# Optimization experiments

Measured on AMD Instinct MI355X. Metric: run time of the kernel, lower is better.

The kernel has to match this reference:

```python
import jax, jax.numpy as jnp
import numpy as np

EPS = 1e-5
N_HEADS = 16

def _bn(x, g, b, m, v):
    # x: (N,C,L); inference-mode batchnorm with running stats
    scale = g * jax.lax.rsqrt(v + EPS)
    return (x - m[None, :, None]) * scale[None, :, None] + b[None, :, None]

def _conv1d(x, w, b, pad):
    # x: (N,C,L), w: (O,I,K) torch layout
    y = jax.lax.conv_general_dilated(x, w, window_strides=(1,), padding=[(pad, pad)],
                                     dimension_numbers=('NCH', 'OIH', 'NCH'))
    return y + b[None, :, None]

def _instance_norm(x):
    m = x.mean(-1, keepdims=True)
    v = x.var(-1, keepdims=True)
    return (x - m) * jax.lax.rsqrt(v + EPS)

def setup_inputs() -> dict:
    key = jax.random.key(0)
    ks = jax.random.split(key, 12)
    C, MID, N, L = 1024, 1024, 4, 1024
    s = 0.02
    d = {
        'x': jax.random.normal(ks[0], (N, C, L), jnp.float32),
        'norm_g': jnp.ones((C,), jnp.float32) + 0.1 * jax.random.normal(ks[1], (C,)),
        'norm_b': 0.1 * jax.random.normal(ks[2], (C,)),
        'norm_m': 0.05 * jax.random.normal(ks[3], (C,)),
        'norm_v': jnp.ones((C,), jnp.float32),
        'wq': s * jax.random.normal(ks[4], (C, C)),
        'wk': s * jax.random.normal(ks[5], (C, C)),
        'wv': s * jax.random.normal(ks[6], (C, C)),
        'wo': s * jax.random.normal(ks[7], (C, C)),
        'cw1': s * jax.random.normal(ks[8], (MID, C, 1)),
        'cb1': jnp.zeros((MID,), jnp.float32),
        'cw2': s * jax.random.normal(ks[9], (MID, MID, 3)),
        'cb2': jnp.zeros((MID,), jnp.float32),
        'cw3': s * jax.random.normal(ks[10], (C, MID, 1)),
        'cb3': jnp.zeros((C,), jnp.float32),
    }
    for i, cdim in [(1, MID), (2, MID), (3, C)]:
        kk = jax.random.split(ks[11], 8)
        d[f'bn{i}_g'] = jnp.ones((cdim,), jnp.float32) + 0.1 * jax.random.normal(kk[2 * i - 2], (cdim,))
        d[f'bn{i}_b'] = 0.1 * jax.random.normal(kk[2 * i - 1], (cdim,))
        d[f'bn{i}_m'] = 0.05 * jax.random.normal(jax.random.fold_in(key, 100 + i), (cdim,))
        d[f'bn{i}_v'] = jnp.ones((cdim,), jnp.float32)
    return d

def _attention(h, wq, wk, wv, wo):
    # h: (N,L,C) ; torch Linear: y = x @ W.T
    N, L, C = h.shape
    dh = C // N_HEADS
    q = (h @ wq.T).reshape(N, L, N_HEADS, dh)
    k = (h @ wk.T).reshape(N, L, N_HEADS, dh)
    v = (h @ wv.T).reshape(N, L, N_HEADS, dh)
    att = jnp.einsum('nqhd,nkhd->nhqk', q, k) / jnp.sqrt(jnp.float32(C))  # note: /sqrt(d_model) as in source
    att = jax.nn.softmax(att, axis=-1)
    o = jnp.einsum('nhqk,nkhd->nqhd', att, v).reshape(N, L, C)
    return o @ wo.T

def _forward(x, norm_g, norm_b, norm_m, norm_v, wq, wk, wv, wo,
             cw1, cb1, bn1_g, bn1_b, bn1_m, bn1_v,
             cw2, cb2, bn2_g, bn2_b, bn2_m, bn2_v,
             cw3, cb3, bn3_g, bn3_b, bn3_m, bn3_v):
    # self-attention branch (dropout is identity in eval)
    h = _bn(x, norm_g, norm_b, norm_m, norm_v).transpose(0, 2, 1)  # (N,L,C)
    h = h + _attention(h, wq, wk, wv, wo)
    h = h.transpose(0, 2, 1)  # (N,C,L)
    # IbnNet (bottleneck conv block + residual + optional InstanceNorm)
    y = jax.nn.relu(_bn(_conv1d(h, cw1, cb1, 0), bn1_g, bn1_b, bn1_m, bn1_v))
    y = jax.nn.relu(_bn(_conv1d(y, cw2, cb2, 1), bn2_g, bn2_b, bn2_m, bn2_v))
    y = _bn(_conv1d(y, cw3, cb3, 0), bn3_g, bn3_b, bn3_m, bn3_v)
    y = jax.nn.relu(_instance_norm(y + h))
    # max_pool1d(kernel=2, stride=2)
    N, C, L = y.shape
    return y.reshape(N, C, L // 2, 2).max(axis=-1)

def reference(x, norm_g, norm_b, norm_m, norm_v, wq, wk, wv, wo,
              cw1, cb1, bn1_g, bn1_b, bn1_m, bn1_v,
              cw2, cb2, bn2_g, bn2_b, bn2_m, bn2_v,
              cw3, cb3, bn3_g, bn3_b, bn3_m, bn3_v):
    return _forward(x, norm_g, norm_b, norm_m, norm_v, wq, wk, wv, wo,
                    cw1, cb1, bn1_g, bn1_b, bn1_m, bn1_v,
                    cw2, cb2, bn2_g, bn2_b, bn2_m, bn2_v,
                    cw3, cb3, bn3_g, bn3_b, bn3_m, bn3_v)
```

## Files before the change

kernel.cpp:

```cpp
#include <hip/hip_runtime.h>
#include <cstdint>
#include <cstddef>


typedef __bf16 bf16_t;
typedef __attribute__((ext_vector_type(8))) __bf16 bf16x8;
typedef __attribute__((ext_vector_type(4))) __bf16 bf16x4;
typedef __attribute__((ext_vector_type(4))) float f32x4;
typedef __attribute__((ext_vector_type(8))) unsigned short u16x8;
typedef __attribute__((address_space(1))) unsigned int gu32;
typedef __attribute__((address_space(3))) unsigned int lu32;

#define EPSF 1e-5f

__device__ __forceinline__ void glds16(const void* g, void* l) {
  __builtin_amdgcn_global_load_lds((gu32*)g, (lu32*)l, 16, 0, 0);
}

__device__ __forceinline__ f32x4 mfma16(bf16x8 a, bf16x8 b, f32x4 c) {
  return __builtin_amdgcn_mfma_f32_16x16x32_bf16(a, b, c, 0, 0, 0);
}

struct BnAll {
  const float *g0, *b0, *m0, *v0;
  const float *g1, *b1, *m1, *v1, *cb1;
  const float *g2, *b2, *m2, *v2, *cb2;
  const float *g3, *b3, *m3, *v3, *cb3;
};
__global__ void bn_consts4_k(BnAll a, float* __restrict__ base) {
  const int sec = blockIdx.x >> 2;
  const int i = (blockIdx.x & 3) * 256 + threadIdx.x;
  const float *g, *b, *m, *v, *cb;
  switch (sec) {
    case 0: g = a.g0; b = a.b0; m = a.m0; v = a.v0; cb = nullptr; break;
    case 1: g = a.g1; b = a.b1; m = a.m1; v = a.v1; cb = a.cb1; break;
    case 2: g = a.g2; b = a.b2; m = a.m2; v = a.v2; cb = a.cb2; break;
    default: g = a.g3; b = a.b3; m = a.m3; v = a.v3; cb = a.cb3; break;
  }
  float s = g[i] * rsqrtf(v[i] + EPSF);
  base[sec * 2048 + i] = s;
  base[sec * 2048 + 1024 + i] = b[i] + ((cb ? cb[i] : 0.f) - m[i]) * s;
}

__global__ __launch_bounds__(256)
void bn_transpose_k(const float* __restrict__ x, const float* __restrict__ sc,
                    const float* __restrict__ sh, bf16_t* __restrict__ H0b) {
  __shared__ float T[32][33];
  const int n = blockIdx.x, c0 = blockIdx.y * 32, l0 = blockIdx.z * 32;
  const int tx = threadIdx.x & 31, ty = threadIdx.x >> 5;
#pragma unroll
  for (int cc = 0; cc < 4; ++cc) {
    int c = c0 + ty + cc * 8;
    float v = x[((size_t)(n * 1024 + c) << 10) + l0 + tx];
    T[ty + cc * 8][tx] = v * sc[c] + sh[c];
  }
  __syncthreads();
#pragma unroll
  for (int cc = 0; cc < 4; ++cc) {
    int l = l0 + ty + cc * 8;
    float v = T[tx][ty + cc * 8];
    H0b[((size_t)(n * 1024 + l) << 10) + c0 + tx] = (bf16_t)v;
  }
}

__global__ void prep_w_k(const float* __restrict__ s0, const float* __restrict__ s1,
                         const float* __restrict__ s2, const float* __restrict__ s3,
                         const float* __restrict__ s4, const float* __restrict__ s5,
                         const float* __restrict__ w2s,
                         bf16_t* __restrict__ d0, bf16_t* __restrict__ d1,
                         bf16_t* __restrict__ d2, bf16_t* __restrict__ d3,
                         bf16_t* __restrict__ d4, bf16_t* __restrict__ d5,
                         bf16_t* __restrict__ w2d) {
  const int b = blockIdx.x;
  if (b < 6144) {
    const int which = b >> 10;
    const int i = (b & 1023) * 256 + threadIdx.x;
    const float* s; bf16_t* d;
    switch (which) {
      case 0: s = s0; d = d0; break;
      case 1: s = s1; d = d1; break;
      case 2: s = s2; d = d2; break;
      case 3: s = s3; d = d3; break;
      case 4: s = s4; d = d4; break;
      default: s = s5; d = d5; break;
    }
    f32x4 v = *(const f32x4*)(s + (size_t)i * 4);
    bf16x4 o;
    o[0] = (bf16_t)v[0]; o[1] = (bf16_t)v[1]; o[2] = (bf16_t)v[2]; o[3] = (bf16_t)v[3];
    *(bf16x4*)(d + (size_t)i * 4) = o;
  } else {
    const int j0 = ((b - 6144) * 256 + (int)threadIdx.x) * 4;
    const int o = j0 / 3072;
    const int r = j0 - o * 3072;
    const int t = r >> 10;
    const int c0 = r & 1023;
    const float* src = w2s + (size_t)o * 3072 + t;
    bf16x4 ov;
#pragma unroll
    for (int e = 0; e < 4; ++e) ov[e] = (bf16_t)src[(c0 + e) * 3];
    *(bf16x4*)(w2d + (size_t)j0) = ov;
  }
}

__global__ void zero_y1p_pads_k(bf16_t* __restrict__ Y1p) {
  int i = blockIdx.x * 256 + threadIdx.x;
  int n = i >> 11, r = (i >> 10) & 1, c = i & 1023;
  Y1p[(size_t)(n * 1026 + (r ? 1025 : 0)) * 1024 + c] = (bf16_t)0.f;
}

__global__ __launch_bounds__(256)
void gemm_nt(const bf16_t* __restrict__ A, const bf16_t* __restrict__ B, int K,
             int lda, int ldb, int aPad, int outPad, int nNT, int qkv,
             const float* __restrict__ bnScale, const float* __restrict__ bnShift,
             int doRelu, const bf16_t* __restrict__ residB,
             bf16_t* __restrict__ outB, float* __restrict__ statS,
             float* __restrict__ statQ) {
  __shared__ __align__(16) bf16_t As[2][128 * 64];
  __shared__ __align__(16) bf16_t Bs[2][64 * 64];
  __shared__ float SrS[2][2][16], SrQ[2][2][16];

  const int bid = blockIdx.x;
  const int wg = (bid & 7) * (gridDim.x >> 3) + (bid >> 3);
  const int mt = wg / nNT, nt = wg - mt * nNT;
  const int tileM = mt * 128, tileN = nt * 64;

  const int tid = threadIdx.x;
  const int lane = tid & 63;
  const int w = tid >> 6, wr = w >> 1, wc = w & 1;
  const int l16 = lane & 15, g = lane >> 4;

  const bf16_t* aSrc[4];
  const bf16_t* bSrc[2];
#pragma unroll
  for (int it = 0; it < 4; ++it) {
    int q = it * 256 + tid, r = q >> 3, s = q & 7;
    int ar = tileM + r;
    if (aPad) ar = (ar >> 10) * 1026 + (ar & 1023);
    aSrc[it] = A + (size_t)ar * lda + ((s ^ (r & 7)) * 8);
  }
#pragma unroll
  for (int it = 0; it < 2; ++it) {
    int q = it * 256 + tid, r = q >> 3, s = q & 7;
    bSrc[it] = B + (size_t)(tileN + r) * ldb + ((s ^ (r & 7)) * 8);
  }

  f32x4 acc[4][2];
#pragma unroll
  for (int m = 0; m < 4; ++m)
#pragma unroll
    for (int n = 0; n < 2; ++n) acc[m][n] = {0.f, 0.f, 0.f, 0.f};

#pragma unroll
  for (int it = 0; it < 4; ++it) glds16(aSrc[it], &As[0][(it * 256 + tid) * 8]);
#pragma unroll
  for (int it = 0; it < 2; ++it) glds16(bSrc[it], &Bs[0][(it * 256 + tid) * 8]);
  __syncthreads();

  int buf = 0;
  for (int k0 = 0; k0 < K; k0 += 64) {
    if (k0 + 64 < K) {
#pragma unroll
      for (int it = 0; it < 4; ++it)
        glds16(aSrc[it] + k0 + 64, &As[buf ^ 1][(it * 256 + tid) * 8]);
#pragma unroll
      for (int it = 0; it < 2; ++it)
        glds16(bSrc[it] + k0 + 64, &Bs[buf ^ 1][(it * 256 + tid) * 8]);
    }
#pragma unroll
    for (int kk = 0; kk < 2; ++kk) {
      bf16x8 af[4], bfr[2];
#pragma unroll
      for (int m = 0; m < 4; ++m) {
        int r = wr * 64 + m * 16 + l16;
        af[m] = *(const bf16x8*)(&As[buf][r * 64 + (((kk * 4 + g) ^ (r & 7)) * 8)]);
      }
#pragma unroll
      for (int n = 0; n < 2; ++n) {
        int r = wc * 32 + n * 16 + l16;
        bfr[n] = *(const bf16x8*)(&Bs[buf][r * 64 + (((kk * 4 + g) ^ (r & 7)) * 8)]);
      }
#pragma unroll
      for (int m = 0; m < 4; ++m)
#pragma unroll
        for (int n = 0; n < 2; ++n) acc[m][n] = mfma16(af[m], bfr[n], acc[m][n]);
    }
    __syncthreads();
    buf ^= 1;
  }

  float sA[2] = {0.f, 0.f}, qA[2] = {0.f, 0.f};
#pragma unroll
  for (int m = 0; m < 4; ++m) {
#pragma unroll
    for (int n = 0; n < 2; ++n) {
#pragma unroll
      for (int j = 0; j < 4; ++j) {
        const int gr = tileM + wr * 64 + m * 16 + g * 4 + j;
        const int gc = tileN + wc * 32 + n * 16 + l16;
        if (qkv) {
          const int which = gc >> 10, c = gc & 1023;
          float v = acc[m][n][j] * (which == 0 ? 0.03125f : 1.f);
          if (which == 2)
            outB[8388608 + ((size_t)(gr >> 10) << 20) + ((size_t)c << 10) + (gr & 1023)] =
                (bf16_t)v;
          else
            outB[(size_t)which * 4194304 + ((size_t)gr << 10) + c] = (bf16_t)v;
        } else {
          float v = acc[m][n][j];
          if (bnScale) v = v * bnScale[gc] + bnShift[gc];
          if (residB) v += (float)residB[((size_t)gr << 10) + gc];
          if (doRelu) v = fmaxf(v, 0.f);
          size_t orow = gr;
          if (outPad) orow = (size_t)((gr >> 10) * 1026 + (gr & 1023) + 1);
          outB[orow * 1024 + gc] = (bf16_t)v;
          if (statS) { sA[n] += v; qA[n] += v * v; }
        }
      }
    }
  }

  if (statS) {
#pragma unroll
    for (int n = 0; n < 2; ++n) {
      sA[n] += __shfl_xor(sA[n], 16); sA[n] += __shfl_xor(sA[n], 32);
      qA[n] += __shfl_xor(qA[n], 16); qA[n] += __shfl_xor(qA[n], 32);
    }
    if (wr == 1 && lane < 16) {
      SrS[wc][0][lane] = sA[0]; SrS[wc][1][lane] = sA[1];
      SrQ[wc][0][lane] = qA[0]; SrQ[wc][1][lane] = qA[1];
    }
    __syncthreads();
    if (wr == 0 && lane < 16) {
      const int z = mt & 7, nb = mt >> 3;
#pragma unroll
      for (int n = 0; n < 2; ++n) {
        const int gc = tileN + wc * 32 + n * 16 + lane;
        statS[z * 4096 + nb * 1024 + gc] = sA[n] + SrS[wc][n][lane];
        statQ[z * 4096 + nb * 1024 + gc] = qA[n] + SrQ[wc][n][lane];
      }
    }
  }
}

__global__ __launch_bounds__(256)
void attn_fwd(const bf16_t* __restrict__ Qb, const bf16_t* __restrict__ Kb,
              const bf16_t* __restrict__ Vt, bf16_t* __restrict__ AO) {
  __shared__ __align__(16) bf16_t Ks[2][64][64];
  __shared__ __align__(16) bf16_t Vs[2][64][64];
  __shared__ __align__(16) bf16_t Ps[4][2][16][64];

  const int bid = blockIdx.x;
  const int xcd = bid & 7, idx = bid >> 3;
  const int head = xcd * 8 + (idx >> 3);
  const int qblk = idx & 7;
  const int n = head >> 4, h = head & 15;

  const int tid = threadIdx.x, lane = tid & 63, w = tid >> 6;
  const int l16 = lane & 15, g = lane >> 4;
  const int qbase = qblk * 128 + w * 32;

  bf16x8 aq[2][2];
#pragma unroll
  for (int s = 0; s < 2; ++s) {
    const size_t qoff = ((size_t)(n * 1024 + qbase + s * 16 + l16) << 10) + h * 64;
    aq[s][0] = *(const bf16x8*)(Qb + qoff + g * 8);
    aq[s][1] = *(const bf16x8*)(Qb + qoff + 32 + g * 8);
  }

  const bf16_t* Khead = Kb + ((size_t)(n * 1024) << 10) + h * 64;
  const bf16_t* Vhead = Vt + ((size_t)n << 20) + ((size_t)(h * 64) << 10);

  f32x4 oa[2][4];
  float psum[2][4];
#pragma unroll
  for (int s = 0; s < 2; ++s)
#pragma unroll
    for (int i = 0; i < 4; ++i) {
      oa[s][i] = {0.f, 0.f, 0.f, 0.f};
      psum[s][i] = 0.f;
    }

#pragma unroll
  for (int it = 0; it < 2; ++it) {
    int q = it * 256 + tid, r = q >> 3, c = q & 7;
    glds16(Khead + ((size_t)r << 10) + ((c ^ (r & 7)) * 8), &Ks[0][r][c * 8]);
    glds16(Vhead + ((size_t)r << 10) + ((c ^ (r & 7)) * 8), &Vs[0][r][c * 8]);
  }
  asm volatile("s_waitcnt vmcnt(0)" ::: "memory");
  __syncthreads();

  int buf = 0;
  for (int t = 0; t < 16; ++t) {
    if (t < 15) {
      const int kv0 = (t + 1) * 64;
#pragma unroll
      for (int it = 0; it < 2; ++it) {
        int q = it * 256 + tid, r = q >> 3, c = q & 7;
        glds16(Khead + ((size_t)(kv0 + r) << 10) + ((c ^ (r & 7)) * 8),
               &Ks[buf ^ 1][r][c * 8]);
        glds16(Vhead + ((size_t)r << 10) + kv0 + ((c ^ (r & 7)) * 8),
               &Vs[buf ^ 1][r][c * 8]);
      }
    }
    bf16x8 kf[8];
#pragma unroll
    for (int nf = 0; nf < 4; ++nf) {
      const int r = nf * 16 + l16;
      kf[2 * nf]     = *(const bf16x8*)(&Ks[buf][r][((g)     ^ (r & 7)) * 8]);
      kf[2 * nf + 1] = *(const bf16x8*)(&Ks[buf][r][((4 + g) ^ (r & 7)) * 8]);
    }
#pragma unroll
    for (int s = 0; s < 2; ++s) {
      f32x4 sc[4];
#pragma unroll
      for (int nf = 0; nf < 4; ++nf) sc[nf] = {0.f, 0.f, 0.f, 0.f};
#pragma unroll
      for (int nf = 0; nf < 4; ++nf) {
        sc[nf] = mfma16(aq[s][0], kf[2 * nf], sc[nf]);
        sc[nf] = mfma16(aq[s][1], kf[2 * nf + 1], sc[nf]);
      }
#pragma unroll
      for (int nf = 0; nf < 4; ++nf)
#pragma unroll
        for (int j = 0; j < 4; ++j) {
          float p = __expf(sc[nf][j]);
          psum[s][j] += p;
          const int row = g * 4 + j;
          const int ch = (nf * 2 + (l16 >> 3)) ^ (row & 7);
          Ps[w][s][row][ch * 8 + (l16 & 7)] = (bf16_t)p;
        }
    }
    bf16x8 vf[8];
#pragma unroll
    for (int nf = 0; nf < 4; ++nf) {
      const int r = nf * 16 + l16;
      vf[2 * nf]     = *(const bf16x8*)(&Vs[buf][r][((g)     ^ (r & 7)) * 8]);
      vf[2 * nf + 1] = *(const bf16x8*)(&Vs[buf][r][((4 + g) ^ (r & 7)) * 8]);
    }
#pragma unroll
    for (int s = 0; s < 2; ++s)
#pragma unroll
      for (int kk = 0; kk < 2; ++kk) {
        const int ch = (kk * 4 + g) ^ (l16 & 7);
        bf16x8 pa = *(const bf16x8*)(&Ps[w][s][l16][ch * 8]);
#pragma unroll
        for (int nf = 0; nf < 4; ++nf)
          oa[s][nf] = mfma16(pa, vf[2 * nf + kk], oa[s][nf]);
      }
    asm volatile("s_waitcnt vmcnt(0)" ::: "memory");
    __syncthreads();
    buf ^= 1;
  }

#pragma unroll
  for (int s = 0; s < 2; ++s)
#pragma unroll
    for (int j = 0; j < 4; ++j) {
      float sv = psum[s][j];
#pragma unroll
      for (int o = 1; o < 16; o <<= 1) sv += __shfl_xor(sv, o);
      psum[s][j] = sv;
    }
#pragma unroll
  for (int s = 0; s < 2; ++s)
#pragma unroll
    for (int nf = 0; nf < 4; ++nf)
#pragma unroll
      for (int j = 0; j < 4; ++j) {
        const int q = qbase + s * 16 + g * 4 + j;
        AO[((size_t)(n * 1024 + q) << 10) + h * 64 + nf * 16 + l16] =
            (bf16_t)(oa[s][nf][j] / psum[s][j]);
      }
}

__global__ __launch_bounds__(256)
void finalize_k(const bf16_t* __restrict__ Z, const float* __restrict__ ps,
                const float* __restrict__ pq, float* __restrict__ out) {
  __shared__ float T[32][33];
  const int n = blockIdx.x, c0 = blockIdx.y * 32, j0 = blockIdx.z * 32;
  const int tx = threadIdx.x & 31, ty = threadIdx.x >> 5;
  const int c = c0 + tx;
  float s = 0.f, q = 0.f;
#pragma unroll
  for (int z = 0; z < 8; ++z) {
    s += ps[z * 4096 + n * 1024 + c];
    q += pq[z * 4096 + n * 1024 + c];
  }
  const float mean = s * (1.f / 1024.f);
  const float var = q * (1.f / 1024.f) - mean * mean;
  const float rstd = rsqrtf(var + EPSF);
#pragma unroll
  for (int jj = 0; jj < 4; ++jj) {
    const int j = j0 + ty + jj * 8;
    float a = (float)Z[((size_t)(n * 1024 + 2 * j) << 10) + c];
    float b = (float)Z[((size_t)(n * 1024 + 2 * j + 1) << 10) + c];
    float v = (fmaxf(a, b) - mean) * rstd;
    T[ty + jj * 8][tx] = fmaxf(v, 0.f);
  }
  __syncthreads();
#pragma unroll
  for (int jj = 0; jj < 4; ++jj)
    out[((size_t)(n * 1024 + c0 + ty + jj * 8) << 9) + j0 + tx] = T[tx][ty + jj * 8];
}

extern "C" void kernel_launch(void* const* d_in, const int* in_sizes, int n_in,
                              void* d_out, int out_size, void* d_ws, size_t ws_size,
                              hipStream_t stream) {
  const float* x      = (const float*)d_in[0];
  const float* norm_g = (const float*)d_in[1];
  const float* norm_b = (const float*)d_in[2];
  const float* norm_m = (const float*)d_in[3];
  const float* norm_v = (const float*)d_in[4];
  const float* wq     = (const float*)d_in[5];
  const float* wk     = (const float*)d_in[6];
  const float* wv     = (const float*)d_in[7];
  const float* wo     = (const float*)d_in[8];
  const float* cw1    = (const float*)d_in[9];
  const float* cb1    = (const float*)d_in[10];
  const float* cw2    = (const float*)d_in[11];
  const float* cb2    = (const float*)d_in[12];
  const float* cw3    = (const float*)d_in[13];
  const float* cb3    = (const float*)d_in[14];
  const float* bn1_g  = (const float*)d_in[15];
  const float* bn1_b  = (const float*)d_in[16];
  const float* bn1_m  = (const float*)d_in[17];
  const float* bn1_v  = (const float*)d_in[18];
  const float* bn2_g  = (const float*)d_in[19];
  const float* bn2_b  = (const float*)d_in[20];
  const float* bn2_m  = (const float*)d_in[21];
  const float* bn2_v  = (const float*)d_in[22];
  const float* bn3_g  = (const float*)d_in[23];
  const float* bn3_b  = (const float*)d_in[24];
  const float* bn3_m  = (const float*)d_in[25];
  const float* bn3_v  = (const float*)d_in[26];

  char* ws = (char*)d_ws;
  const size_t MB = 1024 * 1024;
  bf16_t* Zb  = (bf16_t*)(ws);
  bf16_t* H0b = (bf16_t*)(ws + 32 * MB);
  bf16_t* Y2  = H0b;
  bf16_t* Qb  = (bf16_t*)(ws + 40 * MB);
  bf16_t* Kb  = (bf16_t*)(ws + 48 * MB);
  bf16_t* Vt  = (bf16_t*)(ws + 56 * MB);
  bf16_t* Y1p = Qb;
  bf16_t* AOb = (bf16_t*)(ws + 64 * MB);
  bf16_t* H2b = (bf16_t*)(ws + 72 * MB);
  bf16_t* wqb = (bf16_t*)(ws + 80 * MB);
  bf16_t* wkb = (bf16_t*)(ws + 82 * MB);
  bf16_t* wvb = (bf16_t*)(ws + 84 * MB);
  bf16_t* wob = (bf16_t*)(ws + 86 * MB);
  bf16_t* w1b = (bf16_t*)(ws + 88 * MB);
  bf16_t* w3b = (bf16_t*)(ws + 90 * MB);
  bf16_t* w2b = (bf16_t*)(ws + 92 * MB);
  float* cb   = (float*)(ws + 98 * MB);
  float* sc0 = cb,        * sh0 = cb + 1024;
  float* sc1 = cb + 2048, * sh1 = cb + 3072;
  float* sc2 = cb + 4096, * sh2 = cb + 5120;
  float* sc3 = cb + 6144, * sh3 = cb + 7168;
  float* ps  = cb + 8192;
  float* pq  = ps + 32768;

  BnAll ba = {norm_g, norm_b, norm_m, norm_v,
              bn1_g, bn1_b, bn1_m, bn1_v, cb1,
              bn2_g, bn2_b, bn2_m, bn2_v, cb2,
              bn3_g, bn3_b, bn3_m, bn3_v, cb3};
  bn_consts4_k<<<16, 256, 0, stream>>>(ba, cb);

  bn_transpose_k<<<dim3(4, 32, 32), 256, 0, stream>>>(x, sc0, sh0, H0b);

  prep_w_k<<<9216, 256, 0, stream>>>(wq, wk, wv, wo, cw1, cw3, cw2,
                                     wqb, wkb, wvb, wob, w1b, w3b, w2b);

  gemm_nt<<<1536, 256, 0, stream>>>(H0b, wqb, 1024, 1024, 1024, 0, 0, 48, 1,
                                    nullptr, nullptr, 0, nullptr, Qb,
                                    nullptr, nullptr);

  attn_fwd<<<512, 256, 0, stream>>>(Qb, Kb, Vt, AOb);

  zero_y1p_pads_k<<<32, 256, 0, stream>>>(Y1p);

  gemm_nt<<<512, 256, 0, stream>>>(AOb, wob, 1024, 1024, 1024, 0, 0, 16, 0,
                                   nullptr, nullptr, 0, H0b, H2b,
                                   nullptr, nullptr);
  gemm_nt<<<512, 256, 0, stream>>>(H2b, w1b, 1024, 1024, 1024, 0, 1, 16, 0,
                                   sc1, sh1, 1, nullptr, Y1p,
                                   nullptr, nullptr);
  gemm_nt<<<512, 256, 0, stream>>>(Y1p, w2b, 3072, 1024, 3072, 1, 0, 16, 0,
                                   sc2, sh2, 1, nullptr, Y2,
                                   nullptr, nullptr);
  gemm_nt<<<512, 256, 0, stream>>>(Y2, w3b, 1024, 1024, 1024, 0, 0, 16, 0,
                                   sc3, sh3, 0, H2b, Zb, ps, pq);

  finalize_k<<<dim3(4, 32, 16), 256, 0, stream>>>(Zb, ps, pq, (float*)d_out);
}
```

Baseline: 246.8 us.

## Add dedicated 256x256-tile pipelined QKV GEMM kernel with 8 waves

```diff
diff --git a/kernel.cpp b/kernel.cpp
--- a/kernel.cpp
+++ b/kernel.cpp
@@ -108,9 +108,135 @@
   Y1p[(size_t)(n * 1026 + (r ? 1025 : 0)) * 1024 + c] = (bf16_t)0.f;
 }
 
+__global__ __launch_bounds__(512, 2)
+void gemm_qkv8(const bf16_t* __restrict__ A, const bf16_t* __restrict__ B,
+               bf16_t* __restrict__ out) {
+  __shared__ __align__(16) bf16_t As[2][2][8192];
+  __shared__ __align__(16) bf16_t Bs[2][2][8192];
+
+  const int bid = blockIdx.x;
+  const int wg = (bid & 7) * 24 + (bid >> 3);
+  const int mt = wg / 12, nt = wg - mt * 12;
+  const int tileM = mt * 256, tileN = nt * 256;
+
+  const int tid = threadIdx.x;
+  const int lane = tid & 63;
+  const int w = tid >> 6;
+  const int wm = w >> 2, wn = w & 3;
+  const int l16 = lane & 15, gg = lane >> 4;
+  const int bhalf = wn >> 1, bbase = (wn & 1) * 64;
+
+  const bf16_t* Abase = A + ((size_t)tileM << 10);
+  const bf16_t* Bbase = B + ((size_t)tileN << 10);
+
+#define STG(LDSHALF, GBASE, ROWBASE, KT)                                     \
+  {                                                                          \
+    _Pragma("unroll") for (int rd = 0; rd < 2; ++rd) {                       \
+      int q = rd * 512 + tid; int rr = q >> 3; int ss = q & 7;               \
+      glds16((GBASE) + (((size_t)((ROWBASE) + rr)) << 10) + ((KT) * 64) +    \
+                 ((ss ^ (rr & 7)) * 8),                                      \
+             &(LDSHALF)[q * 8]);                                             \
+    }                                                                        \
+  }
+
+  bf16x8 aF[4][2], b0F[2][2], b1F[2][2];
+  f32x4 acc[8][4];
+#pragma unroll
+  for (int m = 0; m < 8; ++m)
+#pragma unroll
+    for (int n = 0; n < 4; ++n) acc[m][n] = {0.f, 0.f, 0.f, 0.f};
+
+#define READ_A(DB, AG)                                                       \
+  _Pragma("unroll") for (int i = 0; i < 4; ++i)                              \
+  _Pragma("unroll") for (int kk = 0; kk < 2; ++kk) {                         \
+    int row = (AG) * 64 + i * 16 + l16;                                      \
+    aF[i][kk] = *(const bf16x8*)&As[DB][wm][row * 64 +                       \
+                                            (((kk * 4 + gg) ^ (l16 & 7)) * 8)]; \
+  }
+#define READ_B(DB, BG, DEST)                                                 \
+  _Pragma("unroll") for (int jj = 0; jj < 2; ++jj)                           \
+  _Pragma("unroll") for (int kk = 0; kk < 2; ++kk) {                         \
+    int row = bbase + (BG) * 32 + jj * 16 + l16;                             \
+    DEST[jj][kk] = *(const bf16x8*)&Bs[DB][bhalf][row * 64 +                 \
+                                            (((kk * 4 + gg) ^ (l16 & 7)) * 8)]; \
+  }
+#define MMA_Q(AG, BG, BREG)                                                  \
+  __builtin_amdgcn_s_setprio(1);                                             \
+  _Pragma("unroll") for (int i = 0; i < 4; ++i)                              \
+  _Pragma("unroll") for (int jj = 0; jj < 2; ++jj) {                         \
+    acc[(AG)*4 + i][(BG)*2 + jj] =                                           \
+        mfma16(aF[i][0], BREG[jj][0], acc[(AG)*4 + i][(BG)*2 + jj]);         \
+    acc[(AG)*4 + i][(BG)*2 + jj] =                                           \
+        mfma16(aF[i][1], BREG[jj][1], acc[(AG)*4 + i][(BG)*2 + jj]);         \
+  }                                                                          \
+  __builtin_amdgcn_s_setprio(0);
+
+  STG(As[0][0], Abase, 0, 0);
+  STG(As[0][1], Abase, 128, 0);
+  STG(Bs[0][0], Bbase, 0, 0);
+  STG(Bs[0][1], Bbase, 128, 0);
+  STG(Bs[1][0], Bbase, 0, 1);
+  STG(As[1][0], Abase, 0, 1);
+  asm volatile("s_waitcnt vmcnt(4)" ::: "memory");
+  __builtin_amdgcn_s_barrier();
+
+  const int T = 16;
+  for (int t = 0; t < T; ++t) {
+    const int db = t & 1, dn = db ^ 1;
+    READ_A(db, 0);
+    READ_B(db, 0, b0F);
+    if (t + 1 < T) STG(As[dn][1], Abase, 128, t + 1);
+    __builtin_amdgcn_s_barrier();
+    MMA_Q(0, 0, b0F);
+    __builtin_amdgcn_s_barrier();
+    READ_B(db, 1, b1F);
+    if (t + 1 < T) STG(Bs[dn][1], Bbase, 128, t + 1);
+    __builtin_amdgcn_s_barrier();
+    MMA_Q(0, 1, b1F);
+    __builtin_amdgcn_s_barrier();
+    READ_A(db, 1);
+    if (t + 2 < T) STG(Bs[db][0], Bbase, 0, t + 2);
+    __builtin_amdgcn_s_barrier();
+    MMA_Q(1, 1, b1F);
+    __builtin_amdgcn_s_barrier();
+    if (t + 2 < T) STG(As[db][0], Abase, 0, t + 2);
+    if (t < T - 2) {
+      asm volatile("s_waitcnt vmcnt(4)" ::: "memory");
+    } else if (t == T - 2) {
+      asm volatile("s_waitcnt vmcnt(0)" ::: "memory");
+    }
+    __builtin_amdgcn_s_barrier();
+    MMA_Q(1, 0, b0F);
+    __builtin_amdgcn_s_barrier();
+  }
+#undef STG
+#undef READ_A
+#undef READ_B
+#undef MMA_Q
+
+#pragma unroll
+  for (int m = 0; m < 8; ++m) {
+#pragma unroll
+    for (int n = 0; n < 4; ++n) {
+#pragma unroll
+      for (int j = 0; j < 4; ++j) {
+        const int gr = tileM + wm * 128 + m * 16 + gg * 4 + j;
+        const int gc = tileN + wn * 64 + n * 16 + l16;
+        const int which = gc >> 10, c = gc & 1023;
+        float v = acc[m][n][j] * (which == 0 ? 0.03125f : 1.f);
+        if (which == 2)
+          out[8388608 + ((size_t)(gr >> 10) << 20) + ((size_t)c << 10) + (gr & 1023)] =
+              (bf16_t)v;
+        else
+          out[(size_t)which * 4194304 + ((size_t)gr << 10) + c] = (bf16_t)v;
+      }
+    }
+  }
+}
+
 __global__ __launch_bounds__(256)
 void gemm_nt(const bf16_t* __restrict__ A, const bf16_t* __restrict__ B, int K,
-             int lda, int ldb, int aPad, int outPad, int nNT, int qkv,
+             int lda, int ldb, int aPad, int outPad, int nNT,
              const float* __restrict__ bnScale, const float* __restrict__ bnShift,
              int doRelu, const bf16_t* __restrict__ residB,
              bf16_t* __restrict__ outB, float* __restrict__ statS,
@@ -197,24 +323,14 @@
       for (int j = 0; j < 4; ++j) {
         const int gr = tileM + wr * 64 + m * 16 + g * 4 + j;
         const int gc = tileN + wc * 32 + n * 16 + l16;
-        if (qkv) {
-          const int which = gc >> 10, c = gc & 1023;
-          float v = acc[m][n][j] * (which == 0 ? 0.03125f : 1.f);
-          if (which == 2)
-            outB[8388608 + ((size_t)(gr >> 10) << 20) + ((size_t)c << 10) + (gr & 1023)] =
-                (bf16_t)v;
-          else
-            outB[(size_t)which * 4194304 + ((size_t)gr << 10) + c] = (bf16_t)v;
-        } else {
-          float v = acc[m][n][j];
-          if (bnScale) v = v * bnScale[gc] + bnShift[gc];
-          if (residB) v += (float)residB[((size_t)gr << 10) + gc];
-          if (doRelu) v = fmaxf(v, 0.f);
-          size_t orow = gr;
-          if (outPad) orow = (size_t)((gr >> 10) * 1026 + (gr & 1023) + 1);
-          outB[orow * 1024 + gc] = (bf16_t)v;
-          if (statS) { sA[n] += v; qA[n] += v * v; }
-        }
+        float v = acc[m][n][j];
+        if (bnScale) v = v * bnScale[gc] + bnShift[gc];
+        if (residB) v += (float)residB[((size_t)gr << 10) + gc];
+        if (doRelu) v = fmaxf(v, 0.f);
+        size_t orow = gr;
+        if (outPad) orow = (size_t)((gr >> 10) * 1026 + (gr & 1023) + 1);
+        outB[orow * 1024 + gc] = (bf16_t)v;
+        if (statS) { sA[n] += v; qA[n] += v * v; }
       }
     }
   }
@@ -471,24 +587,22 @@
   prep_w_k<<<9216, 256, 0, stream>>>(wq, wk, wv, wo, cw1, cw3, cw2,
                                      wqb, wkb, wvb, wob, w1b, w3b, w2b);
 
-  gemm_nt<<<1536, 256, 0, stream>>>(H0b, wqb, 1024, 1024, 1024, 0, 0, 48, 1,
-                                    nullptr, nullptr, 0, nullptr, Qb,
-                                    nullptr, nullptr);
+  gemm_qkv8<<<192, 512, 0, stream>>>(H0b, wqb, Qb);
 
   attn_fwd<<<512, 256, 0, stream>>>(Qb, Kb, Vt, AOb);
 
   zero_y1p_pads_k<<<32, 256, 0, stream>>>(Y1p);
 
-  gemm_nt<<<512, 256, 0, stream>>>(AOb, wob, 1024, 1024, 1024, 0, 0, 16, 0,
+  gemm_nt<<<512, 256, 0, stream>>>(AOb, wob, 1024, 1024, 1024, 0, 0, 16,
                                    nullptr, nullptr, 0, H0b, H2b,
                                    nullptr, nullptr);
-  gemm_nt<<<512, 256, 0, stream>>>(H2b, w1b, 1024, 1024, 1024, 0, 1, 16, 0,
+  gemm_nt<<<512, 256, 0, stream>>>(H2b, w1b, 1024, 1024, 1024, 0, 1, 16,
                                    sc1, sh1, 1, nullptr, Y1p,
                                    nullptr, nullptr);
-  gemm_nt<<<512, 256, 0, stream>>>(Y1p, w2b, 3072, 1024, 3072, 1, 0, 16, 0,
+  gemm_nt<<<512, 256, 0, stream>>>(Y1p, w2b, 3072, 1024, 3072, 1, 0, 16,
                                    sc2, sh2, 1, nullptr, Y2,
                                    nullptr, nullptr);
-  gemm_nt<<<512, 256, 0, stream>>>(Y2, w3b, 1024, 1024, 1024, 0, 0, 16, 0,
+  gemm_nt<<<512, 256, 0, stream>>>(Y2, w3b, 1024, 1024, 1024, 0, 0, 16,
                                    sc3, sh3, 0, H2b, Zb, ps, pq);
 
   finalize_k<<<dim3(4, 32, 16), 256, 0, stream>>>(Zb, ps, pq, (float*)d_out);
```

Measured after the change: 256.6 us. 4.0% more time.
